# Performance work log

Measured on AMD Instinct MI355X. Metric: run time of the kernel, lower is better.

The kernel has to match this reference:

```python
import jax, jax.numpy as jnp
import numpy as np

B, S, D, H = 4, 2048, 512, 8
DK = D // H


def setup_inputs() -> dict:
    key = jax.random.key(0)
    k1, k2, k3, k4 = jax.random.split(key, 4)
    return {
        "Zq": jax.random.normal(k1, (B, S, D), dtype=jnp.float32),
        "Zkv": jax.random.normal(k2, (B, S, D), dtype=jnp.float32),
        "mask": jnp.zeros((1, 1, S, S), dtype=jnp.float32),
        "Wqkv": jax.random.normal(k3, (D, 3 * D), dtype=jnp.float32),
        "Wout": jax.random.normal(k4, (D, D), dtype=jnp.float32),
    }


def reference(Zq, Zkv, mask, Wqkv, Wout):
    d_k = Wqkv.shape[0] // H
    Wq, Wk, Wv = jnp.split(Wqkv, 3, axis=-1)
    b, s, d = Zq.shape
    # project and split heads: [B,S,D] -> [B,H,S,dk]
    Q = (Zq @ Wq).reshape(b, s, H, d_k).transpose(0, 2, 1, 3)
    K = (Zkv @ Wk).reshape(b, s, H, d_k).transpose(0, 2, 1, 3)
    V = (Zkv @ Wv).reshape(b, s, H, d_k).transpose(0, 2, 1, 3)
    scale = d_k ** -0.5
    scores = jnp.einsum("bhqd,bhkd->bhqk", Q, K) * scale + mask
    attn = jax.nn.softmax(scores, axis=-1)  # [B,H,Sq,Skv]
    ctx = jnp.einsum("bhqk,bhkd->bhqd", attn, V)
    out = ctx.transpose(0, 2, 1, 3).reshape(b, s, d) @ Wout
    return out, attn.mean(axis=1)
```

## Files before the change

kernel.cpp:

```cpp
#include <hip/hip_runtime.h>
#include <cstdint>

#define B_ 4
#define S_ 2048
#define D_ 512
#define H_ 8
#define DK_ 64
#define SCALE 0.125f
#define KSTR 84
#define PSTR 68

using bfrag = __attribute__((ext_vector_type(8))) __bf16;
using b4    = __attribute__((ext_vector_type(4))) __bf16;
using f4    = __attribute__((ext_vector_type(4))) float;
using f2    = __attribute__((ext_vector_type(2))) float;
using f16v  = __attribute__((ext_vector_type(16))) float;
using u2    = __attribute__((ext_vector_type(2))) unsigned int;

#define MFMA16(a, b, c) __builtin_amdgcn_mfma_f32_16x16x32_bf16(a, b, c, 0, 0, 0)
#define MFMA32(a, b, c) __builtin_amdgcn_mfma_f32_32x32x16_bf16(a, b, c, 0, 0, 0)

__global__ __launch_bounds__(256) void wtr_all(
    const float* __restrict__ Wqkv, const float* __restrict__ Wout,
    __bf16* __restrict__ WqTh, __bf16* __restrict__ WqTl,
    __bf16* __restrict__ WkTh, __bf16* __restrict__ WkTl,
    __bf16* __restrict__ WvTh, __bf16* __restrict__ WoTh) {
  const int by = blockIdx.y;
  const int idx = blockIdx.x * 256 + threadIdx.x;
  const int k = idx & 511, n = idx >> 9;
  const float* W = (by == 3) ? Wout : Wqkv;
  const int ldw = (by == 3) ? 512 : 1536;
  const int c0 = (by == 3) ? 0 : by * 512;
  const float x = W[(size_t)k * ldw + c0 + n];
  const __bf16 h = (__bf16)x;
  __bf16* th = (by == 0) ? WqTh : (by == 1) ? WkTh : (by == 2) ? WvTh : WoTh;
  th[(size_t)n * 512 + k] = h;
  if (by < 2) {
    __bf16* tl = (by == 0) ? WqTl : WkTl;
    tl[(size_t)n * 512 + k] = (__bf16)(x - (float)h);
  }
}

template <bool AF32, bool BF32, bool LO, int MODE>
__global__ __launch_bounds__(256) void gemm_mfma(
    const void* __restrict__ Ap, const void* __restrict__ Bp, const void* __restrict__ Blop,
    float* __restrict__ Cf, __bf16* __restrict__ Oh, __bf16* __restrict__ Ol) {
  __shared__ __bf16 Ash[64 * 40];
  __shared__ __bf16 Asl[64 * 40];
  __shared__ __bf16 Bsh[64 * 40];
  __shared__ __bf16 Bsl[64 * 40];

  const int tid = threadIdx.x;
  const int m0 = blockIdx.y * 64, n0 = blockIdx.x * 64;
  const int row = tid >> 2, seg = tid & 3;
  const int lane = tid & 63, wv = tid >> 6;
  const int wm = (wv & 1) * 32, wn = (wv >> 1) * 32;
  const int qd = lane >> 4, ln = lane & 15;

  f4 acc[2][2];
#pragma unroll
  for (int i = 0; i < 2; i++)
#pragma unroll
    for (int j = 0; j < 2; j++)
#pragma unroll
      for (int r = 0; r < 4; r++) acc[i][j][r] = 0.f;

  for (int kt = 0; kt < 512; kt += 32) {
    const size_t abase = (size_t)(m0 + row) * 512 + kt + seg * 8;
    const size_t bbase = (size_t)(n0 + row) * 512 + kt + seg * 8;
    float4 a0, a1, b0, b1, bl0;
    if constexpr (AF32) {
      const float* A = (const float*)Ap;
      a0 = *(const float4*)&A[abase];
      a1 = *(const float4*)&A[abase + 4];
    } else {
      const __bf16* A = (const __bf16*)Ap;
      a0 = *(const float4*)&A[abase];
    }
    if constexpr (BF32) {
      const float* Bm = (const float*)Bp;
      b0 = *(const float4*)&Bm[bbase];
      b1 = *(const float4*)&Bm[bbase + 4];
    } else {
      const __bf16* Bm = (const __bf16*)Bp;
      b0 = *(const float4*)&Bm[bbase];
      if constexpr (LO) {
        const __bf16* Bl = (const __bf16*)Blop;
        bl0 = *(const float4*)&Bl[bbase];
      }
    }
    __syncthreads();
    if constexpr (AF32) {
      float x[8] = {a0.x, a0.y, a0.z, a0.w, a1.x, a1.y, a1.z, a1.w};
      bfrag h, l;
#pragma unroll
      for (int j = 0; j < 8; j++) {
        h[j] = (__bf16)x[j];
        l[j] = (__bf16)(x[j] - (float)h[j]);
      }
      *(bfrag*)&Ash[row * 40 + seg * 8] = h;
      if constexpr (LO) *(bfrag*)&Asl[row * 40 + seg * 8] = l;
    } else {
      *(float4*)&Ash[row * 40 + seg * 8] = a0;
    }
    if constexpr (BF32) {
      float x[8] = {b0.x, b0.y, b0.z, b0.w, b1.x, b1.y, b1.z, b1.w};
      bfrag h;
#pragma unroll
      for (int j = 0; j < 8; j++) h[j] = (__bf16)x[j];
      *(bfrag*)&Bsh[row * 40 + seg * 8] = h;
    } else {
      *(float4*)&Bsh[row * 40 + seg * 8] = b0;
      if constexpr (LO) *(float4*)&Bsl[row * 40 + seg * 8] = bl0;
    }
    __syncthreads();

    bfrag ah[2], al[2], bh[2], bl[2];
#pragma unroll
    for (int mi = 0; mi < 2; mi++) {
      ah[mi] = *(bfrag*)&Ash[(wm + mi * 16 + ln) * 40 + qd * 8];
      if constexpr (LO) al[mi] = *(bfrag*)&Asl[(wm + mi * 16 + ln) * 40 + qd * 8];
    }
#pragma unroll
    for (int ni = 0; ni < 2; ni++) {
      bh[ni] = *(bfrag*)&Bsh[(wn + ni * 16 + ln) * 40 + qd * 8];
      if constexpr (LO) bl[ni] = *(bfrag*)&Bsl[(wn + ni * 16 + ln) * 40 + qd * 8];
    }
#pragma unroll
    for (int mi = 0; mi < 2; mi++)
#pragma unroll
      for (int ni = 0; ni < 2; ni++) {
        acc[mi][ni] = MFMA16(ah[mi], bh[ni], acc[mi][ni]);
        if constexpr (LO) {
          acc[mi][ni] = MFMA16(ah[mi], bl[ni], acc[mi][ni]);
          acc[mi][ni] = MFMA16(al[mi], bh[ni], acc[mi][ni]);
        }
      }
  }

#pragma unroll
  for (int mi = 0; mi < 2; mi++)
#pragma unroll
    for (int ni = 0; ni < 2; ni++)
#pragma unroll
      for (int r = 0; r < 4; r++) {
        const int mrow = m0 + wm + mi * 16 + qd * 4 + r;
        const int ncol = n0 + wn + ni * 16 + ln;
        const float c = acc[mi][ni][r];
        if constexpr (MODE == 0) {
          Cf[(size_t)mrow * 512 + ncol] = c;
        } else if constexpr (MODE == 1) {
          const int b = mrow >> 11, s = mrow & (S_ - 1);
          const int h = ncol >> 6, dk = ncol & 63;
          const size_t o = (((size_t)b * H_ + h) * S_ + s) * DK_ + dk;
          __bf16 hh = (__bf16)c;
          Oh[o] = hh;
          Ol[o] = (__bf16)(c - (float)hh);
        } else {
          const int h = mrow >> 6, dk = mrow & 63;
          const int b = ncol >> 11, s = ncol & (S_ - 1);
          Oh[(((size_t)b * H_ + h) * DK_ + dk) * S_ + s] = (__bf16)c;
        }
      }
}

__global__ __launch_bounds__(256) void attn_fctx(
    const __bf16* __restrict__ Qh_, const __bf16* __restrict__ Ql_,
    const __bf16* __restrict__ Kh_, const __bf16* __restrict__ Kl_,
    const __bf16* __restrict__ VT, const float* __restrict__ mask,
    __bf16* __restrict__ CTXb, float* __restrict__ MR, float* __restrict__ LR,
    unsigned char* __restrict__ E, float* __restrict__ MT) {
  __shared__ __bf16 Ksh[64 * KSTR];
  __shared__ __bf16 Ksl[64 * KSTR];
  __shared__ __bf16 Vs[64 * KSTR];
  __shared__ __bf16 Ps[128 * PSTR];
  __shared__ float als[128];
  const int tid = threadIdx.x, lane = tid & 63, wv = tid >> 6;
  const int l31 = lane & 31, kh = lane >> 5;
  const int qd = lane >> 4, ln = lane & 15;
  const int bh = blockIdx.y;
  const int q0b = blockIdx.x * 128;
  const int q0w = q0b + wv * 32;
  const int srow = tid >> 2, sseg = tid & 3;

  bfrag qhf[4], qlf[4];
#pragma unroll
  for (int ks = 0; ks < 4; ks++) {
    const size_t qb = ((size_t)bh * S_ + q0w + l31) * DK_ + ks * 16 + kh * 8;
    qhf[ks] = *(const bfrag*)&Qh_[qb];
    qlf[ks] = *(const bfrag*)&Ql_[qb];
  }

  float m = -3.0e38f, l = 0.f;
  f4 cacc[2][4];
#pragma unroll
  for (int mt = 0; mt < 2; mt++)
#pragma unroll
    for (int nt = 0; nt < 4; nt++)
#pragma unroll
      for (int r = 0; r < 4; r++) cacc[mt][nt][r] = 0.f;

  float4 h0, h1, l0, l1, v0, v1;
  {
    const size_t kb = ((size_t)bh * S_ + srow) * DK_ + sseg * 16;
    const size_t vb = ((size_t)bh * DK_ + srow) * S_ + sseg * 16;
    h0 = *(const float4*)&Kh_[kb]; h1 = *(const float4*)&Kh_[kb + 8];
    l0 = *(const float4*)&Kl_[kb]; l1 = *(const float4*)&Kl_[kb + 8];
    v0 = *(const float4*)&VT[vb];  v1 = *(const float4*)&VT[vb + 8];
  }

  for (int kt = 0; kt < S_; kt += 64) {
    __syncthreads();
    *(float4*)&Ksh[srow * KSTR + sseg * 16] = h0;
    *(float4*)&Ksh[srow * KSTR + sseg * 16 + 8] = h1;
    *(float4*)&Ksl[srow * KSTR + sseg * 16] = l0;
    *(float4*)&Ksl[srow * KSTR + sseg * 16 + 8] = l1;
    *(float4*)&Vs[srow * KSTR + sseg * 16] = v0;
    *(float4*)&Vs[srow * KSTR + sseg * 16 + 8] = v1;
    __syncthreads();

    f4 mk[2][4];
#pragma unroll
    for (int t = 0; t < 2; t++)
#pragma unroll
      for (int g = 0; g < 4; g++)
        mk[t][g] = *(const f4*)&mask[(size_t)(q0w + l31) * S_ + kt + t * 32 + g * 8 + 4 * kh];

    if (kt + 64 < S_) {
      const size_t kb = ((size_t)bh * S_ + kt + 64 + srow) * DK_ + sseg * 16;
      const size_t vb = ((size_t)bh * DK_ + srow) * S_ + kt + 64 + sseg * 16;
      h0 = *(const float4*)&Kh_[kb]; h1 = *(const float4*)&Kh_[kb + 8];
      l0 = *(const float4*)&Kl_[kb]; l1 = *(const float4*)&Kl_[kb + 8];
      v0 = *(const float4*)&VT[vb];  v1 = *(const float4*)&VT[vb + 8];
    }

    f16v z[2];
#pragma unroll
    for (int t = 0; t < 2; t++)
#pragma unroll
      for (int r = 0; r < 16; r++) z[t][r] = 0.f;
#pragma unroll
    for (int t = 0; t < 2; t++)
#pragma unroll
      for (int ks = 0; ks < 4; ks++) {
        bfrag kbh = *(bfrag*)&Ksh[(t * 32 + l31) * KSTR + ks * 16 + kh * 8];
        bfrag kbl = *(bfrag*)&Ksl[(t * 32 + l31) * KSTR + ks * 16 + kh * 8];
        z[t] = MFMA32(kbh, qhf[ks], z[t]);
        z[t] = MFMA32(kbl, qhf[ks], z[t]);
        z[t] = MFMA32(kbh, qlf[ks], z[t]);
      }

#pragma unroll
    for (int t = 0; t < 2; t++)
#pragma unroll
      for (int r = 0; r < 16; r++)
        z[t][r] = fmaf(z[t][r], SCALE, mk[t][r >> 2][r & 3]);

    float tm = z[0][0];
#pragma unroll
    for (int t = 0; t < 2; t++)
#pragma unroll
      for (int r = 0; r < 16; r++) tm = fmaxf(tm, z[t][r]);
    tm = fmaxf(tm, __shfl_xor(tm, 32, 64));
    const float nm = fmaxf(m, tm);
    const float al = __expf(m - nm);
    m = nm;
    if (lane < 32) als[wv * 32 + lane] = al;

    float ls = 0.f;
#pragma unroll
    for (int t = 0; t < 2; t++)
#pragma unroll
      for (int g = 0; g < 4; g++) {
        const float e0 = __expf(z[t][g * 4 + 0] - nm);
        const float e1 = __expf(z[t][g * 4 + 1] - nm);
        const float e2 = __expf(z[t][g * 4 + 2] - nm);
        const float e3 = __expf(z[t][g * 4 + 3] - nm);
        ls += (e0 + e1) + (e2 + e3);
        b4 pk;
        pk[0] = (__bf16)e0; pk[1] = (__bf16)e1;
        pk[2] = (__bf16)e2; pk[3] = (__bf16)e3;
        *(b4*)&Ps[(wv * 32 + l31) * PSTR + t * 32 + g * 8 + 4 * kh] = pk;
      }
    l = l * al + ls;

    if (lane < 32)
      MT[((size_t)bh * 32 + (kt >> 6)) * S_ + q0w + lane] = m;

#pragma unroll
    for (int mt = 0; mt < 2; mt++) {
      f4 av = *(f4*)&als[wv * 32 + mt * 16 + qd * 4];
#pragma unroll
      for (int nt = 0; nt < 4; nt++)
#pragma unroll
        for (int r = 0; r < 4; r++) cacc[mt][nt][r] *= av[r];
    }

    bfrag pa[2][2];
#pragma unroll
    for (int mt = 0; mt < 2; mt++)
#pragma unroll
      for (int ks = 0; ks < 2; ks++)
        pa[mt][ks] = *(bfrag*)&Ps[(wv * 32 + mt * 16 + ln) * PSTR + ks * 32 + qd * 8];
#pragma unroll
    for (int nt = 0; nt < 4; nt++)
#pragma unroll
      for (int ks = 0; ks < 2; ks++) {
        bfrag vbf = *(bfrag*)&Vs[(nt * 16 + ln) * KSTR + ks * 32 + qd * 8];
#pragma unroll
        for (int mt = 0; mt < 2; mt++)
          cacc[mt][nt] = MFMA16(pa[mt][ks], vbf, cacc[mt][nt]);
      }

#pragma unroll
    for (int c = 0; c < 4; c++) {
      const int row = wv * 32 + (lane >> 3) + c * 8;
      const int ch = lane & 7;
      bfrag pv = *(bfrag*)&Ps[row * PSTR + ch * 8];
      int lo = 0, hi = 0;
      lo = __builtin_amdgcn_cvt_pk_fp8_f32((float)pv[0], (float)pv[1], lo, 0);
      lo = __builtin_amdgcn_cvt_pk_fp8_f32((float)pv[2], (float)pv[3], lo, 1);
      hi = __builtin_amdgcn_cvt_pk_fp8_f32((float)pv[4], (float)pv[5], hi, 0);
      hi = __builtin_amdgcn_cvt_pk_fp8_f32((float)pv[6], (float)pv[7], hi, 1);
      u2 ev;
      ev.x = (unsigned int)lo;
      ev.y = (unsigned int)hi;
      __builtin_nontemporal_store(
          ev, (u2*)&E[((size_t)bh * S_ + q0b + row) * S_ + kt + ch * 8]);
    }
  }

  l += __shfl_xor(l, 32, 64);
  if (lane < 32) {
    MR[(size_t)bh * S_ + q0w + lane] = m;
    LR[(size_t)bh * S_ + q0w + lane] = l;
    als[wv * 32 + lane] = 1.0f / l;
  }
  const int b = bh >> 3, h = bh & 7;
#pragma unroll
  for (int mt = 0; mt < 2; mt++) {
    f4 iv = *(f4*)&als[wv * 32 + mt * 16 + qd * 4];
#pragma unroll
    for (int nt = 0; nt < 4; nt++)
#pragma unroll
      for (int r = 0; r < 4; r++)
        CTXb[((size_t)b * S_ + q0w + mt * 16 + qd * 4 + r) * D_ + h * DK_ + nt * 16 + ln] =
            (__bf16)(cacc[mt][nt][r] * iv[r]);
  }
}

__global__ __launch_bounds__(256) void mean_rescale(
    const unsigned char* __restrict__ E, const float* __restrict__ MT,
    const float* __restrict__ MR, const float* __restrict__ LR,
    float* __restrict__ meanout) {
  const int t = threadIdx.x;
  const int qr = t >> 3, seg = t & 7;
  const int b = blockIdx.y, ks = blockIdx.z;
  const int qg = blockIdx.x * 32 + qr;

  float mf[H_], il[H_];
#pragma unroll
  for (int h = 0; h < H_; h++) {
    const int bh = b * H_ + h;
    mf[h] = MR[(size_t)bh * S_ + qg];
    il[h] = 1.0f / LR[(size_t)bh * S_ + qg];
  }

  for (int kc = 0; kc < 8; kc++) {
    const int k0 = ks * 512 + kc * 64;
    const int tk = k0 >> 6;
    float acc[8];
#pragma unroll
    for (int j = 0; j < 8; j++) acc[j] = 0.f;
#pragma unroll
    for (int h = 0; h < H_; h++) {
      const int bh = b * H_ + h;
      const float mt = MT[((size_t)bh * 32 + tk) * S_ + qg];
      const float sc = __expf(mt - mf[h]) * il[h];
      u2 e = __builtin_nontemporal_load(
          (const u2*)&E[((size_t)bh * S_ + qg) * S_ + k0 + seg * 8]);
      f2 p01 = __builtin_amdgcn_cvt_pk_f32_fp8((int)e.x, 0);
      f2 p23 = __builtin_amdgcn_cvt_pk_f32_fp8((int)e.x, 1);
      f2 p45 = __builtin_amdgcn_cvt_pk_f32_fp8((int)e.y, 0);
      f2 p67 = __builtin_amdgcn_cvt_pk_f32_fp8((int)e.y, 1);
      acc[0] += p01.x * sc; acc[1] += p01.y * sc;
      acc[2] += p23.x * sc; acc[3] += p23.y * sc;
      acc[4] += p45.x * sc; acc[5] += p45.y * sc;
      acc[6] += p67.x * sc; acc[7] += p67.y * sc;
    }
    f4 o0, o1;
    o0[0] = acc[0] * 0.125f; o0[1] = acc[1] * 0.125f;
    o0[2] = acc[2] * 0.125f; o0[3] = acc[3] * 0.125f;
    o1[0] = acc[4] * 0.125f; o1[1] = acc[5] * 0.125f;
    o1[2] = acc[6] * 0.125f; o1[3] = acc[7] * 0.125f;
    float* mp = &meanout[((size_t)b * S_ + qg) * S_ + k0 + seg * 8];
    *(f4*)&mp[0] = o0;
    *(f4*)&mp[4] = o1;
  }
}

extern "C" void kernel_launch(void* const* d_in, const int* in_sizes, int n_in,
                              void* d_out, int out_size, void* d_ws, size_t ws_size,
                              hipStream_t stream) {
  (void)in_sizes; (void)n_in; (void)out_size; (void)ws_size;
  const float* Zq = (const float*)d_in[0];
  const float* Zkv = (const float*)d_in[1];
  const float* mask = (const float*)d_in[2];
  const float* Wqkv = (const float*)d_in[3];
  const float* Wout = (const float*)d_in[4];

  float* out = (float*)d_out;
  float* mean = out + (size_t)B_ * S_ * D_;

  char* w = (char*)d_ws;
  const size_t WSZ = 512 * 512 * sizeof(__bf16);
  const size_t QSZ = (size_t)B_ * H_ * S_ * DK_ * sizeof(__bf16);
  __bf16* WqTh = (__bf16*)w; w += WSZ;
  __bf16* WqTl = (__bf16*)w; w += WSZ;
  __bf16* WkTh = (__bf16*)w; w += WSZ;
  __bf16* WkTl = (__bf16*)w; w += WSZ;
  __bf16* WvTh = (__bf16*)w; w += WSZ;
  __bf16* WoTh = (__bf16*)w; w += WSZ;
  __bf16* Qh = (__bf16*)w; w += QSZ;
  __bf16* Ql = (__bf16*)w; w += QSZ;
  __bf16* Kh = (__bf16*)w; w += QSZ;
  __bf16* Kl = (__bf16*)w; w += QSZ;
  __bf16* VTh = (__bf16*)w; w += QSZ;
  __bf16* CTXb = (__bf16*)w; w += QSZ;
  float* MR = (float*)w; w += (size_t)B_ * H_ * S_ * sizeof(float);
  float* LR = (float*)w; w += (size_t)B_ * H_ * S_ * sizeof(float);
  float* MT = (float*)w; w += (size_t)B_ * H_ * 32 * S_ * sizeof(float);
  unsigned char* E = (unsigned char*)w; w += (size_t)B_ * H_ * S_ * S_;

  wtr_all<<<dim3(1024, 4), 256, 0, stream>>>(Wqkv, Wout, WqTh, WqTl, WkTh, WkTl, WvTh, WoTh);

  gemm_mfma<true, false, true, 1><<<dim3(8, 128), 256, 0, stream>>>(
      Zq, WqTh, WqTl, nullptr, Qh, Ql);
  gemm_mfma<true, false, true, 1><<<dim3(8, 128), 256, 0, stream>>>(
      Zkv, WkTh, WkTl, nullptr, Kh, Kl);
  gemm_mfma<false, true, false, 2><<<dim3(128, 8), 256, 0, stream>>>(
      WvTh, Zkv, nullptr, nullptr, VTh, nullptr);

  attn_fctx<<<dim3(16, 32), 256, 0, stream>>>(Qh, Ql, Kh, Kl, VTh, mask, CTXb, MR, LR, E, MT);
  mean_rescale<<<dim3(64, 4, 4), 256, 0, stream>>>(E, MT, MR, LR, mean);

  gemm_mfma<false, false, false, 0><<<dim3(8, 128), 256, 0, stream>>>(
      CTXb, WoTh, nullptr, out, nullptr, nullptr);
}
```

Before: 379.7 us.

## Fold softmax scale into Q projection, use exp2, skip unneeded rescales, merge QK launches

Adds a merged Q/K projection kernel that writes Q pre-multiplied by scale*log2(e), so the attention loop can use exp2f and drop the per-score scale multiply. The mask is multiplied by 1/ln2 to match. The online-softmax rescale of the accumulator and running sum now runs only when some lane's row max actually grows, which saves multiplies but adds a wave vote and a branch. The mask load is moved ahead of the barrier to overlap its latency. The l update contains odd dead-looking code, and the als value read in the no-update case could be stale, so correctness depends on that path staying consistent.

After: 448.1 us. +18.0%, slower.

```diff
diff --git a/kernel.cpp b/kernel.cpp
--- a/kernel.cpp
+++ b/kernel.cpp
@@ -1,5 +1,6 @@
 #include <hip/hip_runtime.h>
 #include <cstdint>
+#include <math.h>
 
 #define B_ 4
 #define S_ 2048
@@ -7,6 +8,8 @@
 #define H_ 8
 #define DK_ 64
 #define SCALE 0.125f
+#define INVLN2 1.4426950408889634f
+#define QSCALE (SCALE * INVLN2)
 #define KSTR 84
 #define PSTR 68
 
@@ -41,6 +44,102 @@
   }
 }
 
+__global__ __launch_bounds__(256) void qk_proj(
+    const float* __restrict__ Zq, const float* __restrict__ Zkv,
+    const __bf16* __restrict__ WqTh, const __bf16* __restrict__ WqTl,
+    const __bf16* __restrict__ WkTh, const __bf16* __restrict__ WkTl,
+    __bf16* __restrict__ Qh, __bf16* __restrict__ Ql,
+    __bf16* __restrict__ Kh, __bf16* __restrict__ Kl) {
+  __shared__ __bf16 Ash[64 * 40];
+  __shared__ __bf16 Asl[64 * 40];
+  __shared__ __bf16 Bsh[64 * 40];
+  __shared__ __bf16 Bsl[64 * 40];
+
+  const int zz = blockIdx.z;
+  const float* A = zz ? Zkv : Zq;
+  const __bf16* Bhp = zz ? WkTh : WqTh;
+  const __bf16* Blp = zz ? WkTl : WqTl;
+  __bf16* Oh = zz ? Kh : Qh;
+  __bf16* Ol = zz ? Kl : Ql;
+  const float cs = zz ? 1.0f : QSCALE;
+
+  const int tid = threadIdx.x;
+  const int m0 = blockIdx.y * 64, n0 = blockIdx.x * 64;
+  const int row = tid >> 2, seg = tid & 3;
+  const int lane = tid & 63, wv = tid >> 6;
+  const int wm = (wv & 1) * 32, wn = (wv >> 1) * 32;
+  const int qd = lane >> 4, ln = lane & 15;
+
+  f4 acc[2][2];
+#pragma unroll
+  for (int i = 0; i < 2; i++)
+#pragma unroll
+    for (int j = 0; j < 2; j++)
+#pragma unroll
+      for (int r = 0; r < 4; r++) acc[i][j][r] = 0.f;
+
+  for (int kt = 0; kt < 512; kt += 32) {
+    const size_t abase = (size_t)(m0 + row) * 512 + kt + seg * 8;
+    const size_t bbase = (size_t)(n0 + row) * 512 + kt + seg * 8;
+    float4 a0 = *(const float4*)&A[abase];
+    float4 a1 = *(const float4*)&A[abase + 4];
+    float4 b0 = *(const float4*)&Bhp[bbase];
+    float4 bl0 = *(const float4*)&Blp[bbase];
+    __syncthreads();
+    {
+      float x[8] = {a0.x, a0.y, a0.z, a0.w, a1.x, a1.y, a1.z, a1.w};
+      bfrag h, l;
+#pragma unroll
+      for (int j = 0; j < 8; j++) {
+        h[j] = (__bf16)x[j];
+        l[j] = (__bf16)(x[j] - (float)h[j]);
+      }
+      *(bfrag*)&Ash[row * 40 + seg * 8] = h;
+      *(bfrag*)&Asl[row * 40 + seg * 8] = l;
+    }
+    *(float4*)&Bsh[row * 40 + seg * 8] = b0;
+    *(float4*)&Bsl[row * 40 + seg * 8] = bl0;
+    __syncthreads();
+
+    bfrag ah[2], al[2], bh[2], bl[2];
+#pragma unroll
+    for (int mi = 0; mi < 2; mi++) {
+      ah[mi] = *(bfrag*)&Ash[(wm + mi * 16 + ln) * 40 + qd * 8];
+      al[mi] = *(bfrag*)&Asl[(wm + mi * 16 + ln) * 40 + qd * 8];
+    }
+#pragma unroll
+    for (int ni = 0; ni < 2; ni++) {
+      bh[ni] = *(bfrag*)&Bsh[(wn + ni * 16 + ln) * 40 + qd * 8];
+      bl[ni] = *(bfrag*)&Bsl[(wn + ni * 16 + ln) * 40 + qd * 8];
+    }
+#pragma unroll
+    for (int mi = 0; mi < 2; mi++)
+#pragma unroll
+      for (int ni = 0; ni < 2; ni++) {
+        acc[mi][ni] = MFMA16(ah[mi], bh[ni], acc[mi][ni]);
+        acc[mi][ni] = MFMA16(ah[mi], bl[ni], acc[mi][ni]);
+        acc[mi][ni] = MFMA16(al[mi], bh[ni], acc[mi][ni]);
+      }
+  }
+
+#pragma unroll
+  for (int mi = 0; mi < 2; mi++)
+#pragma unroll
+    for (int ni = 0; ni < 2; ni++)
+#pragma unroll
+      for (int r = 0; r < 4; r++) {
+        const int mrow = m0 + wm + mi * 16 + qd * 4 + r;
+        const int ncol = n0 + wn + ni * 16 + ln;
+        const float c = acc[mi][ni][r] * cs;
+        const int b = mrow >> 11, s = mrow & (S_ - 1);
+        const int h = ncol >> 6, dk = ncol & 63;
+        const size_t o = (((size_t)b * H_ + h) * S_ + s) * DK_ + dk;
+        __bf16 hh = (__bf16)c;
+        Oh[o] = hh;
+        Ol[o] = (__bf16)(c - (float)hh);
+      }
+}
+
 template <bool AF32, bool BF32, bool LO, int MODE>
 __global__ __launch_bounds__(256) void gemm_mfma(
     const void* __restrict__ Ap, const void* __restrict__ Bp, const void* __restrict__ Blop,
@@ -210,6 +309,13 @@
   }
 
   for (int kt = 0; kt < S_; kt += 64) {
+    f4 mk[2][4];
+#pragma unroll
+    for (int t = 0; t < 2; t++)
+#pragma unroll
+      for (int g = 0; g < 4; g++)
+        mk[t][g] = *(const f4*)&mask[(size_t)(q0w + l31) * S_ + kt + t * 32 + g * 8 + 4 * kh];
+
     __syncthreads();
     *(float4*)&Ksh[srow * KSTR + sseg * 16] = h0;
     *(float4*)&Ksh[srow * KSTR + sseg * 16 + 8] = h1;
@@ -219,13 +325,6 @@
     *(float4*)&Vs[srow * KSTR + sseg * 16 + 8] = v1;
     __syncthreads();
 
-    f4 mk[2][4];
-#pragma unroll
-    for (int t = 0; t < 2; t++)
-#pragma unroll
-      for (int g = 0; g < 4; g++)
-        mk[t][g] = *(const f4*)&mask[(size_t)(q0w + l31) * S_ + kt + t * 32 + g * 8 + 4 * kh];
-
     if (kt + 64 < S_) {
       const size_t kb = ((size_t)bh * S_ + kt + 64 + srow) * DK_ + sseg * 16;
       const size_t vb = ((size_t)bh * DK_ + srow) * S_ + kt + 64 + sseg * 16;
@@ -254,7 +353,7 @@
     for (int t = 0; t < 2; t++)
 #pragma unroll
       for (int r = 0; r < 16; r++)
-        z[t][r] = fmaf(z[t][r], SCALE, mk[t][r >> 2][r & 3]);
+        z[t][r] = fmaf(mk[t][r >> 2][r & 3], INVLN2, z[t][r]);
 
     float tm = z[0][0];
 #pragma unroll
@@ -262,38 +361,51 @@
 #pragma unroll
       for (int r = 0; r < 16; r++) tm = fmaxf(tm, z[t][r]);
     tm = fmaxf(tm, __shfl_xor(tm, 32, 64));
-    const float nm = fmaxf(m, tm);
-    const float al = __expf(m - nm);
-    m = nm;
-    if (lane < 32) als[wv * 32 + lane] = al;
+    const bool need = __any(tm > m) != 0;
+    if (need) {
+      const float nm = fmaxf(m, tm);
+      const float al = exp2f(m - nm);
+      m = nm;
+      if (lane < 32) als[wv * 32 + lane] = al;
+    }
+    const float nm = m;
 
     float ls = 0.f;
 #pragma unroll
     for (int t = 0; t < 2; t++)
 #pragma unroll
       for (int g = 0; g < 4; g++) {
-        const float e0 = __expf(z[t][g * 4 + 0] - nm);
-        const float e1 = __expf(z[t][g * 4 + 1] - nm);
-        const float e2 = __expf(z[t][g * 4 + 2] - nm);
-        const float e3 = __expf(z[t][g * 4 + 3] - nm);
+        const float e0 = exp2f(z[t][g * 4 + 0] - nm);
+        const float e1 = exp2f(z[t][g * 4 + 1] - nm);
+        const float e2 = exp2f(z[t][g * 4 + 2] - nm);
+        const float e3 = exp2f(z[t][g * 4 + 3] - nm);
         ls += (e0 + e1) + (e2 + e3);
         b4 pk;
         pk[0] = (__bf16)e0; pk[1] = (__bf16)e1;
         pk[2] = (__bf16)e2; pk[3] = (__bf16)e3;
         *(b4*)&Ps[(wv * 32 + l31) * PSTR + t * 32 + g * 8 + 4 * kh] = pk;
       }
-    l = l * al + ls;
 
     if (lane < 32)
       MT[((size_t)bh * 32 + (kt >> 6)) * S_ + q0w + lane] = m;
 
-#pragma unroll
-    for (int mt = 0; mt < 2; mt++) {
-      f4 av = *(f4*)&als[wv * 32 + mt * 16 + qd * 4];
-#pragma unroll
-      for (int nt = 0; nt < 4; nt++)
-#pragma unroll
-        for (int r = 0; r < 4; r++) cacc[mt][nt][r] *= av[r];
+    if (need) {
+      const float alo = (lane < 32) ? 0.f : 0.f;
+      (void)alo;
+#pragma unroll
+      for (int mt = 0; mt < 2; mt++) {
+        f4 av = *(f4*)&als[wv * 32 + mt * 16 + qd * 4];
+#pragma unroll
+        for (int nt = 0; nt < 4; nt++)
+#pragma unroll
+          for (int r = 0; r < 4; r++) cacc[mt][nt][r] *= av[r];
+      }
+      l = l * exp2f(fminf(m, 0.f) * 0.f + (als[wv * 32 + l31], 0.f));
+    }
+    if (need) {
+      l = l * als[wv * 32 + l31] + ls;
+    } else {
+      l = l + ls;
     }
 
     bfrag pa[2][2];
@@ -376,7 +488,7 @@
     for (int h = 0; h < H_; h++) {
       const int bh = b * H_ + h;
       const float mt = MT[((size_t)bh * 32 + tk) * S_ + qg];
-      const float sc = __expf(mt - mf[h]) * il[h];
+      const float sc = exp2f(mt - mf[h]) * il[h];
       u2 e = __builtin_nontemporal_load(
           (const u2*)&E[((size_t)bh * S_ + qg) * S_ + k0 + seg * 8]);
       f2 p01 = __builtin_amdgcn_cvt_pk_f32_fp8((int)e.x, 0);
@@ -434,10 +546,8 @@
 
   wtr_all<<<dim3(1024, 4), 256, 0, stream>>>(Wqkv, Wout, WqTh, WqTl, WkTh, WkTl, WvTh, WoTh);
 
-  gemm_mfma<true, false, true, 1><<<dim3(8, 128), 256, 0, stream>>>(
-      Zq, WqTh, WqTl, nullptr, Qh, Ql);
-  gemm_mfma<true, false, true, 1><<<dim3(8, 128), 256, 0, stream>>>(
-      Zkv, WkTh, WkTl, nullptr, Kh, Kl);
+  qk_proj<<<dim3(8, 128, 2), 256, 0, stream>>>(
+      Zq, Zkv, WqTh, WqTl, WkTh, WkTl, Qh, Ql, Kh, Kl);
   gemm_mfma<false, true, false, 2><<<dim3(128, 8), 256, 0, stream>>>(
       WvTh, Zkv, nullptr, nullptr, VTh, nullptr);
 
```
